# Kernel optimization log

Hardware: AMD Instinct MI355X
Metric: run time of the kernel (lower is better)

## Reference

```python
import jax, jax.numpy as jnp
import numpy as np
from jax import lax

EPS = 1e-6
NUM_BANDS = 128


def setup_inputs() -> dict:
    key = jax.random.key(0)
    kx, = jax.random.split(key, 1)
    B, C, F, T = 32, 1, NUM_BANDS, 6000
    x = jax.random.uniform(kx, (B, C, F, T), dtype=jnp.float32)  # nonneg spectrogram energies
    # parameters per band, initialized as in PCEN.__init__ (s=0.025, alpha=delta=r=1.0)
    log_s = jnp.full((F,), np.log(0.025), dtype=jnp.float32)
    log_alpha = jnp.zeros((F,), dtype=jnp.float32)
    log_delta = jnp.zeros((F,), dtype=jnp.float32)
    log_r = jnp.zeros((F,), dtype=jnp.float32)
    return {"x": x, "log_s": log_s, "log_alpha": log_alpha,
            "log_delta": log_delta, "log_r": log_r}


def _pcen(x, log_s, log_alpha, log_delta, log_r):
    # x: (B, C, bands, T)
    s = jnp.exp(log_s)  # (bands,)
    xt = jnp.moveaxis(x, -1, 0)  # (T, B, C, bands) time-major for the scan
    init = xt[0]  # init_smoother_from_data=True -> M_0 = X_0

    def step(m, xf):
        m_new = (1.0 - s) * m + s * xf
        return m_new, m_new

    _, ms = lax.scan(step, init, xt[1:])  # (T-1, B, C, bands)
    smoother = jnp.concatenate([init[None], ms], axis=0)  # (T, B, C, bands)
    smoother = jnp.moveaxis(smoother, 0, -1)  # (B, C, bands, T)

    alpha = jnp.exp(log_alpha)[:, None]  # (bands, 1)
    delta = jnp.exp(log_delta)[:, None]
    r = jnp.exp(log_r)[:, None]
    # (eps + M)^(-alpha) computed stably: exp(-alpha * (log eps + log1p(M/eps)))
    gain = jnp.exp(-alpha * (jnp.log(EPS) + jnp.log1p(smoother / EPS)))
    return (x * gain + delta) ** r - delta ** r


def reference(x, log_s, log_alpha, log_delta, log_r):
    return _pcen(x, log_s, log_alpha, log_delta, log_r)
```

## Files before the change

kernel.cpp:

```cpp
#include <hip/hip_runtime.h>

#define TLEN   6000
#define NV4    1500
#define V4PT   4
#define EPT    16
#define NTILES 6
#define EPS    1e-6f
#define LN_EPS (-13.815511f)
#define INV_EPS 1e6f

__device__ __forceinline__ float pcen_full(float xv, float M, float alpha,
                                           float delta, float r, float deltar) {
    float gain = __expf(-alpha * (LN_EPS + __logf(fmaf(M, INV_EPS, 1.0f))));
    return __powf(fmaf(xv, gain, delta), r) - deltar;
}

__global__ __launch_bounds__(256, 4) void pcen_kernel(
    const float* __restrict__ x,
    const float* __restrict__ log_s,
    const float* __restrict__ log_alpha,
    const float* __restrict__ log_delta,
    const float* __restrict__ log_r,
    float* __restrict__ out,
    int num_series, int F)
{
    const int wave = (int)((blockIdx.x * blockDim.x + threadIdx.x) >> 6);
    const int lane = (int)(threadIdx.x & 63);
    if (wave >= num_series) return;

    const int f = wave % F;

    const float la = log_alpha[f], ld = log_delta[f], lr = log_r[f];
    const bool  triv = (la == 0.0f) && (ld == 0.0f) && (lr == 0.0f);

    const float s   = __expf(log_s[f]);
    const float oms = 1.0f - s;

    float pw[EPT + 1];
    pw[0] = 1.0f;
    #pragma unroll
    for (int k = 1; k <= EPT; ++k) pw[k] = pw[k - 1] * oms;
    const float oms4 = pw[4];

    const float alpha  = __expf(la);
    const float delta  = __expf(ld);
    const float r      = __expf(lr);
    const float deltar = __powf(delta, r);

    const float4* __restrict__ xb = (const float4*)(x + (size_t)wave * TLEN);
    float4* __restrict__ ob       = (float4*)(out + (size_t)wave * TLEN);

    float Mc = 0.0f;

    float4 q[V4PT];
    {
        const int tb = 4 * lane;
        #pragma unroll
        for (int j = 0; j < V4PT; ++j)
            q[j] = (tb + j < NV4) ? xb[tb + j] : make_float4(0.f, 0.f, 0.f, 0.f);
    }

    for (int tile = 0; tile < NTILES; ++tile) {
        const int tb = tile * 256 + 4 * lane;

        float4 p[V4PT];
        #pragma unroll
        for (int j = 0; j < V4PT; ++j) p[j] = make_float4(0.f, 0.f, 0.f, 0.f);
        if (tile + 1 < NTILES) {
            const int nb = tb + 256;
            #pragma unroll
            for (int j = 0; j < V4PT; ++j)
                if (nb + j < NV4) p[j] = xb[nb + j];
        }

        float Bv[EPT];
        float B = 0.0f, A = 1.0f;
        #pragma unroll
        for (int j = 0; j < V4PT; ++j) {
            const bool ok = (tb + j) < NV4;
            if (ok) {
                const float4 xq = q[j];
                const float c0 = (tile == 0 && lane == 0 && j == 0) ? 1.0f : s;
                B = fmaf(oms, B, c0 * xq.x); Bv[4 * j + 0] = B;
                B = fmaf(oms, B, s  * xq.y); Bv[4 * j + 1] = B;
                B = fmaf(oms, B, s  * xq.z); Bv[4 * j + 2] = B;
                B = fmaf(oms, B, s  * xq.w); Bv[4 * j + 3] = B;
                A *= oms4;
            }
        }

        #pragma unroll
        for (int off = 1; off < 64; off <<= 1) {
            const float Ap = __shfl_up(A, off, 64);
            const float Bp = __shfl_up(B, off, 64);
            if (lane >= off) { B = fmaf(A, Bp, B); A = A * Ap; }
        }
        const float A63 = __shfl(A, 63, 64);
        const float B63 = __shfl(B, 63, 64);
        float Ae = __shfl_up(A, 1, 64);
        float Be = __shfl_up(B, 1, 64);
        if (lane == 0) { Ae = 1.0f; Be = 0.0f; }

        const float Min = fmaf(Ae, Mc, Be);

        if (triv) {
            #pragma unroll
            for (int j = 0; j < V4PT; ++j) {
                if ((tb + j) < NV4) {
                    const float4 xq = q[j];
                    float4 o;
                    float m;
                    m = fmaf(pw[4 * j + 1], Min, Bv[4 * j + 0]);
                    o.x = xq.x * __builtin_amdgcn_rcpf(m + EPS);
                    m = fmaf(pw[4 * j + 2], Min, Bv[4 * j + 1]);
                    o.y = xq.y * __builtin_amdgcn_rcpf(m + EPS);
                    m = fmaf(pw[4 * j + 3], Min, Bv[4 * j + 2]);
                    o.z = xq.z * __builtin_amdgcn_rcpf(m + EPS);
                    m = fmaf(pw[4 * j + 4], Min, Bv[4 * j + 3]);
                    o.w = xq.w * __builtin_amdgcn_rcpf(m + EPS);
                    ob[tb + j] = o;
                }
            }
        } else {
            #pragma unroll
            for (int j = 0; j < V4PT; ++j) {
                if ((tb + j) < NV4) {
                    const float4 xq = q[j];
                    float4 o;
                    float m;
                    m = fmaf(pw[4 * j + 1], Min, Bv[4 * j + 0]);
                    o.x = pcen_full(xq.x, m, alpha, delta, r, deltar);
                    m = fmaf(pw[4 * j + 2], Min, Bv[4 * j + 1]);
                    o.y = pcen_full(xq.y, m, alpha, delta, r, deltar);
                    m = fmaf(pw[4 * j + 3], Min, Bv[4 * j + 2]);
                    o.z = pcen_full(xq.z, m, alpha, delta, r, deltar);
                    m = fmaf(pw[4 * j + 4], Min, Bv[4 * j + 3]);
                    o.w = pcen_full(xq.w, m, alpha, delta, r, deltar);
                    ob[tb + j] = o;
                }
            }
        }

        Mc = fmaf(A63, Mc, B63);
        #pragma unroll
        for (int j = 0; j < V4PT; ++j) q[j] = p[j];
    }
}

extern "C" void kernel_launch(void* const* d_in, const int* in_sizes, int n_in,
                              void* d_out, int out_size, void* d_ws, size_t ws_size,
                              hipStream_t stream) {
    const float* x         = (const float*)d_in[0];
    const float* log_s     = (const float*)d_in[1];
    const float* log_alpha = (const float*)d_in[2];
    const float* log_delta = (const float*)d_in[3];
    const float* log_r     = (const float*)d_in[4];
    float* out             = (float*)d_out;

    const int F = in_sizes[1];
    const int num_series = in_sizes[0] / TLEN;
    const int waves_per_block = 4;
    const int grid = (num_series + waves_per_block - 1) / waves_per_block;

    pcen_kernel<<<grid, 256, 0, stream>>>(x, log_s, log_alpha, log_delta, log_r,
                                          out, num_series, F);
}
```

Baseline: 200.0 us.

## Split each time series into parallel chunks with decayed warm-up carry

Instead of one wave scanning all six tiles of a series serially, each of six waves handles one chunk and recomputes the incoming smoother state from the previous chunk via a weighted reduction. With s=0.025 the carry from earlier chunks decays below 1e-7, so only the immediately preceding chunk is re-read when decay_ok holds. This raises the wave count sixfold to expose more parallelism and shorten the serial dependency chain. The cost is re-reading one extra chunk per wave, which adds roughly 5/6 more input loads.

Result: faster. 187.1 us (-6.5%).

```diff
diff --git a/kernel.cpp b/kernel.cpp
--- a/kernel.cpp
+++ b/kernel.cpp
@@ -1,18 +1,30 @@
 #include <hip/hip_runtime.h>
 
-#define TLEN   6000
-#define NV4    1500
-#define V4PT   4
-#define EPT    16
-#define NTILES 6
-#define EPS    1e-6f
-#define LN_EPS (-13.815511f)
-#define INV_EPS 1e6f
+#define TLEN     6000
+#define NV4      1500
+#define CHUNK_V4 256
+#define NCHUNK   6
+#define V4PL     4
+#define EPT      16
+#define EPS      1e-6f
+#define LN_EPS   (-13.815511f)
+#define INV_EPS  1e6f
 
 __device__ __forceinline__ float pcen_full(float xv, float M, float alpha,
                                            float delta, float r, float deltar) {
     float gain = __expf(-alpha * (LN_EPS + __logf(fmaf(M, INV_EPS, 1.0f))));
     return __powf(fmaf(xv, gain, delta), r) - deltar;
+}
+
+__device__ __forceinline__ float ipow6(float b, int e) {
+    float r = 1.0f;
+    #pragma unroll
+    for (int i = 0; i < 6; ++i) {
+        if (e & 1) r *= b;
+        b *= b;
+        e >>= 1;
+    }
+    return r;
 }
 
 __global__ __launch_bounds__(256, 4) void pcen_kernel(
@@ -24,126 +36,154 @@
     float* __restrict__ out,
     int num_series, int F)
 {
-    const int wave = (int)((blockIdx.x * blockDim.x + threadIdx.x) >> 6);
+    const int g    = (int)((blockIdx.x * blockDim.x + threadIdx.x) >> 6);
     const int lane = (int)(threadIdx.x & 63);
-    if (wave >= num_series) return;
-
-    const int f = wave % F;
+    if (g >= num_series * NCHUNK) return;
+    const int series = g / NCHUNK;
+    const int c      = g - series * NCHUNK;
+    const int f      = series % F;
 
     const float la = log_alpha[f], ld = log_delta[f], lr = log_r[f];
     const bool  triv = (la == 0.0f) && (ld == 0.0f) && (lr == 0.0f);
 
-    const float s   = __expf(log_s[f]);
-    const float oms = 1.0f - s;
+    const float s    = __expf(log_s[f]);
+    const float oms  = 1.0f - s;
 
     float pw[EPT + 1];
     pw[0] = 1.0f;
     #pragma unroll
     for (int k = 1; k <= EPT; ++k) pw[k] = pw[k - 1] * oms;
-    const float oms4 = pw[4];
+    const float oms4  = pw[4];
+    const float omsP  = pw[16];
+
+    float A_chunk = omsP;
+    #pragma unroll
+    for (int i = 0; i < 6; ++i) A_chunk *= A_chunk;
+    const bool decay_ok = fabsf(A_chunk) < 1e-7f;
+
+    const float wl = ipow6(omsP, 63 - lane);
 
     const float alpha  = __expf(la);
     const float delta  = __expf(ld);
     const float r      = __expf(lr);
-    const float deltar = __powf(delta, r);
-
-    const float4* __restrict__ xb = (const float4*)(x + (size_t)wave * TLEN);
-    float4* __restrict__ ob       = (float4*)(out + (size_t)wave * TLEN);
+    const float deltar = __powf(delta, lr == 0.0f ? 1.0f : r);
+
+    const float4* __restrict__ xb = (const float4*)(x + (size_t)series * TLEN);
+    float4* __restrict__ ob       = (float4*)(out + (size_t)series * TLEN);
+
+    const int tb = c * CHUNK_V4 + 4 * lane;
+    const int wb = (c - 1) * CHUNK_V4 + 4 * lane;
+    float4 wq[V4PL], q[V4PL];
+    if (c > 0) {
+        #pragma unroll
+        for (int j = 0; j < V4PL; ++j) wq[j] = xb[wb + j];
+    }
+    #pragma unroll
+    for (int j = 0; j < V4PL; ++j)
+        q[j] = (tb + j < NV4) ? xb[tb + j] : make_float4(0.f, 0.f, 0.f, 0.f);
 
     float Mc = 0.0f;
 
-    float4 q[V4PT];
-    {
-        const int tb = 4 * lane;
-        #pragma unroll
-        for (int j = 0; j < V4PT; ++j)
-            q[j] = (tb + j < NV4) ? xb[tb + j] : make_float4(0.f, 0.f, 0.f, 0.f);
-    }
-
-    for (int tile = 0; tile < NTILES; ++tile) {
-        const int tb = tile * 256 + 4 * lane;
-
-        float4 p[V4PT];
-        #pragma unroll
-        for (int j = 0; j < V4PT; ++j) p[j] = make_float4(0.f, 0.f, 0.f, 0.f);
-        if (tile + 1 < NTILES) {
-            const int nb = tb + 256;
+    if (!decay_ok) {
+        for (int wc = 0; wc + 1 < c; ++wc) {
+            const int b0 = wc * CHUNK_V4 + 4 * lane;
+            float B = 0.0f;
             #pragma unroll
-            for (int j = 0; j < V4PT; ++j)
-                if (nb + j < NV4) p[j] = xb[nb + j];
-        }
-
-        float Bv[EPT];
-        float B = 0.0f, A = 1.0f;
-        #pragma unroll
-        for (int j = 0; j < V4PT; ++j) {
-            const bool ok = (tb + j) < NV4;
-            if (ok) {
+            for (int j = 0; j < V4PL; ++j) {
+                const float4 xq = xb[b0 + j];
+                const float c0 = (wc == 0 && lane == 0 && j == 0) ? 1.0f : s;
+                B = fmaf(oms, B, c0 * xq.x);
+                B = fmaf(oms, B, s  * xq.y);
+                B = fmaf(oms, B, s  * xq.z);
+                B = fmaf(oms, B, s  * xq.w);
+            }
+            float v = wl * B;
+            #pragma unroll
+            for (int off = 1; off < 64; off <<= 1)
+                v += __shfl_xor(v, off, 64);
+            Mc = fmaf(A_chunk, Mc, v);
+        }
+    }
+
+    if (c > 0) {
+        float B = 0.0f;
+        #pragma unroll
+        for (int j = 0; j < V4PL; ++j) {
+            const float4 xq = wq[j];
+            const float c0 = (c == 1 && lane == 0 && j == 0) ? 1.0f : s;
+            B = fmaf(oms, B, c0 * xq.x);
+            B = fmaf(oms, B, s  * xq.y);
+            B = fmaf(oms, B, s  * xq.z);
+            B = fmaf(oms, B, s  * xq.w);
+        }
+        float v = wl * B;
+        #pragma unroll
+        for (int off = 1; off < 64; off <<= 1)
+            v += __shfl_xor(v, off, 64);
+        Mc = fmaf(A_chunk, Mc, v);
+    }
+
+    float Bv[EPT];
+    float B = 0.0f, A = 1.0f;
+    #pragma unroll
+    for (int j = 0; j < V4PL; ++j) {
+        if (tb + j < NV4) {
+            const float4 xq = q[j];
+            const float c0 = (c == 0 && lane == 0 && j == 0) ? 1.0f : s;
+            B = fmaf(oms, B, c0 * xq.x); Bv[4 * j + 0] = B;
+            B = fmaf(oms, B, s  * xq.y); Bv[4 * j + 1] = B;
+            B = fmaf(oms, B, s  * xq.z); Bv[4 * j + 2] = B;
+            B = fmaf(oms, B, s  * xq.w); Bv[4 * j + 3] = B;
+            A *= oms4;
+        }
+    }
+
+    #pragma unroll
+    for (int off = 1; off < 64; off <<= 1) {
+        const float Ap = __shfl_up(A, off, 64);
+        const float Bp = __shfl_up(B, off, 64);
+        if (lane >= off) { B = fmaf(A, Bp, B); A = A * Ap; }
+    }
+    float Ae = __shfl_up(A, 1, 64);
+    float Be = __shfl_up(B, 1, 64);
+    if (lane == 0) { Ae = 1.0f; Be = 0.0f; }
+
+    const float Min = fmaf(Ae, Mc, Be);
+
+    if (triv) {
+        #pragma unroll
+        for (int j = 0; j < V4PL; ++j) {
+            if (tb + j < NV4) {
                 const float4 xq = q[j];
-                const float c0 = (tile == 0 && lane == 0 && j == 0) ? 1.0f : s;
-                B = fmaf(oms, B, c0 * xq.x); Bv[4 * j + 0] = B;
-                B = fmaf(oms, B, s  * xq.y); Bv[4 * j + 1] = B;
-                B = fmaf(oms, B, s  * xq.z); Bv[4 * j + 2] = B;
-                B = fmaf(oms, B, s  * xq.w); Bv[4 * j + 3] = B;
-                A *= oms4;
+                float4 o; float m;
+                m = fmaf(pw[4 * j + 1], Min, Bv[4 * j + 0]);
+                o.x = xq.x * __builtin_amdgcn_rcpf(m + EPS);
+                m = fmaf(pw[4 * j + 2], Min, Bv[4 * j + 1]);
+                o.y = xq.y * __builtin_amdgcn_rcpf(m + EPS);
+                m = fmaf(pw[4 * j + 3], Min, Bv[4 * j + 2]);
+                o.z = xq.z * __builtin_amdgcn_rcpf(m + EPS);
+                m = fmaf(pw[4 * j + 4], Min, Bv[4 * j + 3]);
+                o.w = xq.w * __builtin_amdgcn_rcpf(m + EPS);
+                ob[tb + j] = o;
             }
         }
-
-        #pragma unroll
-        for (int off = 1; off < 64; off <<= 1) {
-            const float Ap = __shfl_up(A, off, 64);
-            const float Bp = __shfl_up(B, off, 64);
-            if (lane >= off) { B = fmaf(A, Bp, B); A = A * Ap; }
-        }
-        const float A63 = __shfl(A, 63, 64);
-        const float B63 = __shfl(B, 63, 64);
-        float Ae = __shfl_up(A, 1, 64);
-        float Be = __shfl_up(B, 1, 64);
-        if (lane == 0) { Ae = 1.0f; Be = 0.0f; }
-
-        const float Min = fmaf(Ae, Mc, Be);
-
-        if (triv) {
-            #pragma unroll
-            for (int j = 0; j < V4PT; ++j) {
-                if ((tb + j) < NV4) {
-                    const float4 xq = q[j];
-                    float4 o;
-                    float m;
-                    m = fmaf(pw[4 * j + 1], Min, Bv[4 * j + 0]);
-                    o.x = xq.x * __builtin_amdgcn_rcpf(m + EPS);
-                    m = fmaf(pw[4 * j + 2], Min, Bv[4 * j + 1]);
-                    o.y = xq.y * __builtin_amdgcn_rcpf(m + EPS);
-                    m = fmaf(pw[4 * j + 3], Min, Bv[4 * j + 2]);
-                    o.z = xq.z * __builtin_amdgcn_rcpf(m + EPS);
-                    m = fmaf(pw[4 * j + 4], Min, Bv[4 * j + 3]);
-                    o.w = xq.w * __builtin_amdgcn_rcpf(m + EPS);
-                    ob[tb + j] = o;
-                }
+    } else {
+        #pragma unroll
+        for (int j = 0; j < V4PL; ++j) {
+            if (tb + j < NV4) {
+                const float4 xq = q[j];
+                float4 o; float m;
+                m = fmaf(pw[4 * j + 1], Min, Bv[4 * j + 0]);
+                o.x = pcen_full(xq.x, m, alpha, delta, r, deltar);
+                m = fmaf(pw[4 * j + 2], Min, Bv[4 * j + 1]);
+                o.y = pcen_full(xq.y, m, alpha, delta, r, deltar);
+                m = fmaf(pw[4 * j + 3], Min, Bv[4 * j + 2]);
+                o.z = pcen_full(xq.z, m, alpha, delta, r, deltar);
+                m = fmaf(pw[4 * j + 4], Min, Bv[4 * j + 3]);
+                o.w = pcen_full(xq.w, m, alpha, delta, r, deltar);
+                ob[tb + j] = o;
             }
-        } else {
-            #pragma unroll
-            for (int j = 0; j < V4PT; ++j) {
-                if ((tb + j) < NV4) {
-                    const float4 xq = q[j];
-                    float4 o;
-                    float m;
-                    m = fmaf(pw[4 * j + 1], Min, Bv[4 * j + 0]);
-                    o.x = pcen_full(xq.x, m, alpha, delta, r, deltar);
-                    m = fmaf(pw[4 * j + 2], Min, Bv[4 * j + 1]);
-                    o.y = pcen_full(xq.y, m, alpha, delta, r, deltar);
-                    m = fmaf(pw[4 * j + 3], Min, Bv[4 * j + 2]);
-                    o.z = pcen_full(xq.z, m, alpha, delta, r, deltar);
-                    m = fmaf(pw[4 * j + 4], Min, Bv[4 * j + 3]);
-                    o.w = pcen_full(xq.w, m, alpha, delta, r, deltar);
-                    ob[tb + j] = o;
-                }
-            }
-        }
-
-        Mc = fmaf(A63, Mc, B63);
-        #pragma unroll
-        for (int j = 0; j < V4PT; ++j) q[j] = p[j];
+        }
     }
 }
 
@@ -159,8 +199,9 @@
 
     const int F = in_sizes[1];
     const int num_series = in_sizes[0] / TLEN;
-    const int waves_per_block = 4;
-    const int grid = (num_series + waves_per_block - 1) / waves_per_block;
+    const int num_waves  = num_series * NCHUNK;
+    const int num_threads = num_waves * 64;
+    const int grid = (num_threads + 255) / 256;
 
     pcen_kernel<<<grid, 256, 0, stream>>>(x, log_s, log_alpha, log_delta, log_r,
                                           out, num_series, F);
```
